# Kernel optimization log

Measured on AMD Instinct MI355X. Metric: run time of the kernel, lower is better.

Reference implementation:

```python
import jax, jax.numpy as jnp
import numpy as np

N_V = 250        # n_vertices (hardcoded in module)
NUM_WS = 14
W_DIM = 512
Z_DIM = 512
B = 64
E_PER = 1488     # ~directed convex-hull edges per graph (3N-6 undirected)
LR = 0.01        # lr_multiplier
CAM_R = 1.3


def _fc(x, w, b):
    # StyleGAN FullyConnectedLayer: runtime weight gain lr/sqrt(fan_in), bias gain lr,
    # bias_act 'lrelu' (alpha=0.2) with gain sqrt(2).
    gain = LR / np.sqrt(w.shape[1])
    y = x @ (w.T * gain) + b * LR
    return jax.nn.leaky_relu(y, 0.2) * np.sqrt(2.0)


def _seg_mean(vals, idx, n):
    s = jax.ops.segment_sum(vals, idx, num_segments=n)
    c = jax.ops.segment_sum(jnp.ones((idx.shape[0], 1), vals.dtype), idx, num_segments=n)
    return s / jnp.maximum(c, 1.0)


def _processor(x, edge_index, edge_attr, ew0, eb0, ew1, eb1, nw0, nb0, nw1, nb1, out_dim):
    src, dst = edge_index[0], edge_index[1]
    # edge encoder on [x_recv, x_send, edge_attr]
    ef = jnp.concatenate([x[src], x[dst], edge_attr], axis=-1)
    ef = _fc(_fc(ef, ew0, eb0), ew1, eb1)
    # PyG propagate (flow source_to_target): message = cat([x_i, edge_attr]) with
    # x_i = x[edge_index[1]], mean-aggregated onto edge_index[1].
    msg = jnp.concatenate([x[dst], ef], axis=-1)
    agg = _seg_mean(msg, dst, x.shape[0])
    nf = jnp.concatenate([x, agg[:, out_dim:]], axis=-1)
    nf = _fc(_fc(nf, nw0, nb0), nw1, nb1)
    return nf, ef


def setup_inputs() -> dict:
    key = jax.random.key(0)
    ks = jax.random.split(key, 24)
    z = jax.random.normal(ks[0], (B, Z_DIM), jnp.float32)
    la = jax.random.normal(ks[1], (B * N_V, 3), jnp.float32)
    look_ats = -CAM_R * la / jnp.linalg.norm(la, axis=-1, keepdims=True)
    # block-structured edges: each graph's edges stay within its 250-node block
    rng = np.random.default_rng(0)
    base = np.repeat(np.arange(B, dtype=np.int32) * N_V, E_PER)
    src = base + rng.integers(0, N_V, size=B * E_PER).astype(np.int32)
    dst = base + rng.integers(0, N_V, size=B * E_PER).astype(np.int32)
    edge_index = jnp.asarray(np.stack([src, dst]))
    # FullyConnectedLayer weights: init N(0,1)/lr_multiplier, bias 0
    def w(k, o, i):
        return jax.random.normal(k, (o, i), jnp.float32) / LR
    D = W_DIM
    inp = dict(z=z, look_ats=look_ats, edge_index=edge_index)
    inp.update(
        p0_ew0=w(ks[2], D, 1034), p0_eb0=jnp.zeros((D,), jnp.float32),
        p0_ew1=w(ks[3], D, D),    p0_eb1=jnp.zeros((D,), jnp.float32),
        p0_nw0=w(ks[4], D, 1030), p0_nb0=jnp.zeros((D,), jnp.float32),
        p0_nw1=w(ks[5], D, D),    p0_nb1=jnp.zeros((D,), jnp.float32),
        p1_ew0=w(ks[6], D, 1536), p1_eb0=jnp.zeros((D,), jnp.float32),
        p1_ew1=w(ks[7], D, D),    p1_eb1=jnp.zeros((D,), jnp.float32),
        p1_nw0=w(ks[8], D, 1024), p1_nb0=jnp.zeros((D,), jnp.float32),
        p1_nw1=w(ks[9], D, D),    p1_nb1=jnp.zeros((D,), jnp.float32),
    )
    return inp


def reference(z, look_ats, edge_index,
              p0_ew0, p0_eb0, p0_ew1, p0_eb1, p0_nw0, p0_nb0, p0_nw1, p0_nb1,
              p1_ew0, p1_eb0, p1_ew1, p1_eb1, p1_nw0, p1_nb0, p1_nw1, p1_nb1):
    b = z.shape[0]
    # normalize_2nd_moment
    zn = z * jax.lax.rsqrt(jnp.mean(jnp.square(z), axis=-1, keepdims=True) + 1e-8)
    # generate_graph: x = cat([z.repeat(N,1), look_ats]); edge_attr from look_ats
    x = jnp.concatenate([jnp.tile(zn, (N_V, 1)), look_ats], axis=-1)  # [B*N, 515]
    rel = look_ats[edge_index[1]] - look_ats[edge_index[0]]
    dist = jnp.linalg.norm(rel, axis=-1, keepdims=True)
    ea = jnp.concatenate([rel, dist], axis=-1)  # [E, 4]
    x, ea = _processor(x, edge_index, ea, p0_ew0, p0_eb0, p0_ew1, p0_eb1,
                       p0_nw0, p0_nb0, p0_nw1, p0_nb1, W_DIM)
    x, ea = _processor(x, edge_index, ea, p1_ew0, p1_eb0, p1_ew1, p1_eb1,
                       p1_nw0, p1_nb0, p1_nw1, p1_nb1, W_DIM)
    ws = x[::N_V]                        # in_ids = [i*N for i in range(B)]
    return jnp.tile(ws[:, None, :], (1, NUM_WS, 1))  # [B, num_ws, w_dim]
```

## Files before the change

kernel.cpp:

```cpp
#include <hip/hip_runtime.h>
#include <hip/hip_bf16.h>
#include <cmath>

#define NVP 250
#define NN  16000
#define EN  95232
#define LRc 0.01f
#define SQ2 1.41421356237309515f

#define CAP_ES 1024
#define CAP_N1 1024
#define CAP_E0 4096
#define EBLK ((EN + 255) / 256)
#define NBLK ((NN + 255) / 256)
#define SK_T 4

typedef __attribute__((ext_vector_type(8))) short bf16x8;
typedef __attribute__((ext_vector_type(4))) float f32x4;

__device__ __forceinline__ unsigned short bfc(float x) {
  unsigned u = __builtin_bit_cast(unsigned, x);
  u = (u + 0x7fffu + ((u >> 16) & 1u)) >> 16;
  return (unsigned short)u;
}
__device__ __forceinline__ unsigned pk2(float a, float b) {
  return (unsigned)bfc(a) | ((unsigned)bfc(b) << 16);
}

struct FEP {
  const float* bias; float gain;
  const float* T0p; const float* la; const float* cnt; const float* w0n;
  const int* rmap; const int* dst; const int* posN;
  float* outp; float* atomp;
};

template<int EPI>
__device__ __forceinline__ void mfma_epi(const FEP& f, f32x4 acc0, f32x4 acc1,
                                         f32x4 acc2, f32x4 acc3,
                                         int mBase, int nBase, int M,
                                         int lane, int wv) {
  const int fcol = lane & 15;
  int rows[4]; bool rok[4]; int tr[4];
  int rr4[4]; float la0[4], la1[4], la2[4]; bool has[4];
#pragma unroll
  for (int r = 0; r < 4; r++) {
    int row = mBase + wv*16 + (lane >> 4)*4 + r;
    rows[r] = row; rok[r] = row < M;
    int rc = rok[r] ? row : 0;
    if (EPI == 1) tr[r] = f.posN[f.dst[f.rmap[rc]]];
    if (EPI == 2) tr[r] = f.dst[f.rmap[rc]] / NVP;
    if (EPI == 7) {
      int nd = f.rmap[rc];
      rr4[r] = nd & 63;
      la0[r] = f.la[nd*3]; la1[r] = f.la[nd*3+1]; la2[r] = f.la[nd*3+2];
      has[r] = f.cnt[nd] > 0.f;
    }
  }
  f32x4 accs[4] = {acc0, acc1, acc2, acc3};
#pragma unroll
  for (int c = 0; c < 4; c++) {
    int n = nBase + fcol + 16*c;
    float bi = f.bias[n] * LRc;
    float w6[6];
    if (EPI == 7) {
#pragma unroll
      for (int j = 0; j < 6; j++) w6[j] = f.w0n[j*512 + n];
    }
#pragma unroll
    for (int r = 0; r < 4; r++) {
      if (!rok[r]) continue;
      float yr = accs[c][r];
      if (EPI == 7) {
#pragma unroll
        for (int zz = 0; zz < SK_T; zz++)
          yr += f.T0p[((size_t)zz*64 + rr4[r])*512 + n];
        float corr = la0[r]*w6[0] + la1[r]*w6[1] + la2[r]*w6[2];
        if (has[r]) corr += la0[r]*w6[3] + la1[r]*w6[4] + la2[r]*w6[5];
        yr += corr;
      }
      float y = yr * f.gain + bi;
      y = (y > 0.f ? y : 0.2f*y) * SQ2;
      if (EPI == 0 || EPI == 7) {
        f.outp[(size_t)rows[r]*512 + n] = y;
      } else if (EPI == 1) {
        f.outp[(size_t)rows[r]*512 + n] = y;
        atomicAdd(&f.atomp[(size_t)tr[r]*512 + n], y);
      } else {
        atomicAdd(&f.atomp[(size_t)tr[r]*512 + n], y);
      }
    }
  }
}

struct GMF {
  const float* W; const float* Ain; const int* Mdev;
  const float* cnt; const int* listN1;
  int Wld, Woff, Astride, K, Mcap, Mfix;
  FEP f;
};

template<int VECW, int SCALED, int EPI>
__global__ __launch_bounds__(256) void gemmMF(GMF p) {
  int M = p.Mdev ? *p.Mdev : p.Mfix;
  if (M > p.Mcap) M = p.Mcap;
  const int mBase = blockIdx.x * 64;
  if (mBase >= M) return;
  const int nBase = blockIdx.y * 64;

  __shared__ unsigned short Abf[64*72];
  __shared__ unsigned short Wbf[64*72];
  const int t = threadIdx.x;
  const int srow = t >> 2, sq = (t & 3) * 16;
  int arow = mBase + srow; if (arow >= M) arow = M - 1;
  float s = 1.f;
  if (SCALED) s = 1.0f / fmaxf(p.cnt[p.listN1[arow]], 1.0f);
  const float* aRow = p.Ain + (size_t)arow * p.Astride + sq;
  const float* wRow = p.W + (size_t)(nBase + srow) * p.Wld + p.Woff + sq;

  float4 ra[4], rw[4];
  auto ld = [&](int kt) {
#pragma unroll
    for (int i = 0; i < 4; i++) {
      ra[i] = *(const float4*)(aRow + kt + 4*i);
      if (VECW) {
        rw[i] = *(const float4*)(wRow + kt + 4*i);
      } else {
        const float* wp = wRow + kt + 4*i;
        rw[i] = make_float4(wp[0], wp[1], wp[2], wp[3]);
      }
    }
  };
  ld(0);

  const int lane = t & 63, wv = t >> 6;
  const int fr = wv*16 + (lane & 15);
  const int fcol = (lane & 15);
  const int fo = (lane >> 4) * 8;
  f32x4 acc0 = {}, acc1 = {}, acc2 = {}, acc3 = {};

  for (int kt = 0; kt < p.K; kt += 64) {
    if (kt > 0) __syncthreads();
    unsigned short* da = &Abf[srow*72 + sq];
    unsigned short* dw = &Wbf[srow*72 + sq];
#pragma unroll
    for (int i = 0; i < 4; i++) {
      uint2 ua; ua.x = pk2(ra[i].x*s, ra[i].y*s); ua.y = pk2(ra[i].z*s, ra[i].w*s);
      *(uint2*)&da[i*4] = ua;
      uint2 uw; uw.x = pk2(rw[i].x, rw[i].y); uw.y = pk2(rw[i].z, rw[i].w);
      *(uint2*)&dw[i*4] = uw;
    }
    __syncthreads();
    if (kt + 64 < p.K) ld(kt + 64);
#pragma unroll
    for (int kk = 0; kk < 64; kk += 32) {
      bf16x8 a = *(const bf16x8*)&Abf[fr*72 + kk + fo];
      bf16x8 b0 = *(const bf16x8*)&Wbf[( 0 + fcol)*72 + kk + fo];
      bf16x8 b1 = *(const bf16x8*)&Wbf[(16 + fcol)*72 + kk + fo];
      bf16x8 b2 = *(const bf16x8*)&Wbf[(32 + fcol)*72 + kk + fo];
      bf16x8 b3 = *(const bf16x8*)&Wbf[(48 + fcol)*72 + kk + fo];
      acc0 = __builtin_amdgcn_mfma_f32_16x16x32_bf16(a, b0, acc0, 0, 0, 0);
      acc1 = __builtin_amdgcn_mfma_f32_16x16x32_bf16(a, b1, acc1, 0, 0, 0);
      acc2 = __builtin_amdgcn_mfma_f32_16x16x32_bf16(a, b2, acc2, 0, 0, 0);
      acc3 = __builtin_amdgcn_mfma_f32_16x16x32_bf16(a, b3, acc3, 0, 0, 0);
    }
  }
  mfma_epi<EPI>(p.f, acc0, acc1, acc2, acc3, mBase, nBase, M, lane, wv);
}

struct GGS {
  const float* W; const float* x1c; const float* ef0c;
  const int* listES; const int* src; const int* dst; const int* posN; const int* posOf;
  const int* Mdev; float* pbuf; int KC;
};
__global__ __launch_bounds__(256) void gemmGS(GGS p) {
  int M = *p.Mdev; if (M > CAP_ES) M = CAP_ES;
  const int mBase = blockIdx.x * 64;
  if (mBase >= M) return;
  const int nBase = blockIdx.y * 64;
  const int z = blockIdx.z;
  int kBeg = z * p.KC, kEnd = kBeg + p.KC;

  __shared__ unsigned short Abf[64*72];
  __shared__ unsigned short Wbf[64*72];
  const int t = threadIdx.x;
  const int srow = t >> 2, sq = (t & 3) * 16;
  int arow = mBase + srow; if (arow >= M) arow = M - 1;
  int e = p.listES[arow];
  const float* s0 = p.x1c + (size_t)p.posN[p.src[e]] * 512;
  const float* s1 = p.x1c + (size_t)p.posN[p.dst[e]] * 512;
  const float* s2 = p.ef0c + (size_t)p.posOf[e] * 512;
  const float* wRow = p.W + (size_t)(nBase + srow) * 1536 + sq;

  float4 ra[4], rw[4];
  auto ld = [&](int kt) {
    int ka = kt + sq;
    const float* ap = (ka < 512) ? (s0 + ka) : (ka < 1024) ? (s1 + ka - 512)
                                                           : (s2 + ka - 1024);
#pragma unroll
    for (int i = 0; i < 4; i++) {
      ra[i] = *(const float4*)(ap + 4*i);
      rw[i] = *(const float4*)(wRow + kt + 4*i);
    }
  };
  ld(kBeg);

  const int lane = t & 63, wv = t >> 6;
  const int fr = wv*16 + (lane & 15);
  const int fcol = (lane & 15);
  const int fo = (lane >> 4) * 8;
  f32x4 acc0 = {}, acc1 = {}, acc2 = {}, acc3 = {};

  for (int kt = kBeg; kt < kEnd; kt += 64) {
    if (kt > kBeg) __syncthreads();
    unsigned short* da = &Abf[srow*72 + sq];
    unsigned short* dw = &Wbf[srow*72 + sq];
#pragma unroll
    for (int i = 0; i < 4; i++) {
      uint2 ua; ua.x = pk2(ra[i].x, ra[i].y); ua.y = pk2(ra[i].z, ra[i].w);
      *(uint2*)&da[i*4] = ua;
      uint2 uw; uw.x = pk2(rw[i].x, rw[i].y); uw.y = pk2(rw[i].z, rw[i].w);
      *(uint2*)&dw[i*4] = uw;
    }
    __syncthreads();
    if (kt + 64 < kEnd) ld(kt + 64);
#pragma unroll
    for (int kk = 0; kk < 64; kk += 32) {
      bf16x8 a = *(const bf16x8*)&Abf[fr*72 + kk + fo];
      bf16x8 b0 = *(const bf16x8*)&Wbf[( 0 + fcol)*72 + kk + fo];
      bf16x8 b1 = *(const bf16x8*)&Wbf[(16 + fcol)*72 + kk + fo];
      bf16x8 b2 = *(const bf16x8*)&Wbf[(32 + fcol)*72 + kk + fo];
      bf16x8 b3 = *(const bf16x8*)&Wbf[(48 + fcol)*72 + kk + fo];
      acc0 = __builtin_amdgcn_mfma_f32_16x16x32_bf16(a, b0, acc0, 0, 0, 0);
      acc1 = __builtin_amdgcn_mfma_f32_16x16x32_bf16(a, b1, acc1, 0, 0, 0);
      acc2 = __builtin_amdgcn_mfma_f32_16x16x32_bf16(a, b2, acc2, 0, 0, 0);
      acc3 = __builtin_amdgcn_mfma_f32_16x16x32_bf16(a, b3, acc3, 0, 0, 0);
    }
  }
  float* ob = p.pbuf + (size_t)z * CAP_ES * 512;
  int orow = mBase + wv*16 + (lane >> 4) * 4;
  int oc = nBase + fcol;
#pragma unroll
  for (int r = 0; r < 4; r++) {
    float* q = ob + (size_t)(orow + r) * 512 + oc;
    q[0] = acc0[r]; q[16] = acc1[r]; q[32] = acc2[r]; q[48] = acc3[r];
  }
}

struct EPS {
  const float* pbuf; const float* bias; const int* Mdev;
  float* outp; int SK; float gain;
};
__global__ __launch_bounds__(256) void epiS_k(EPS e) {
  int M = *e.Mdev; if (M > CAP_ES) M = CAP_ES;
  int i = blockIdx.x*256 + threadIdx.x;
  if (i >= M*128) return;
  int m = i >> 7, n4 = (i & 127) * 4;
  float ys[4] = {0.f, 0.f, 0.f, 0.f};
  for (int z = 0; z < e.SK; z++) {
    float4 v = *(const float4*)&e.pbuf[((size_t)z*CAP_ES + m)*512 + n4];
    ys[0] += v.x; ys[1] += v.y; ys[2] += v.z; ys[3] += v.w;
  }
#pragma unroll
  for (int j = 0; j < 4; j++) {
    float y = ys[j] * e.gain + e.bias[n4+j] * LRc;
    ys[j] = (y > 0.f ? y : 0.2f*y) * SQ2;
  }
  *(float4*)&e.outp[(size_t)m*512 + n4] = make_float4(ys[0],ys[1],ys[2],ys[3]);
}

template<int VECW, int NSEG>
__device__ __forceinline__ void gemm_loop(
    const float* const* b0, const float* const* b1,
    const float* sc0, const float* sc1,
    const float* w0, const float* w1, const float* w2, const float* w3,
    int kBeg, int kEnd,
    float (*As)[36], float (*Bs)[68], float acc[4][4]) {
  const int t = threadIdx.x;
  const int k4 = (t & 7) * 4;
  const int mr = t >> 3;
  const int tx = t & 15, ty = t >> 4;
  float4 ra0, ra1, rw0, rw1, rw2, rw3;
  auto lA = [&](int k0) {
    int ka = k0 + k4;
    int idx = 0;
    if (NSEG >= 2 && ka >= 512) idx = 1;
    if (NSEG == 3 && ka >= 1024) idx = 2;
    float s0 = sc0[idx], s1 = sc1[idx];
    ra0 = *(const float4*)(b0[idx] + ka);
    ra1 = *(const float4*)(b1[idx] + ka);
    ra0.x *= s0; ra0.y *= s0; ra0.z *= s0; ra0.w *= s0;
    ra1.x *= s1; ra1.y *= s1; ra1.z *= s1; ra1.w *= s1;
  };
  auto lW = [&](int k0) {
    if (VECW) {
      rw0 = *(const float4*)(w0 + k0); rw1 = *(const float4*)(w1 + k0);
      rw2 = *(const float4*)(w2 + k0); rw3 = *(const float4*)(w3 + k0);
    } else {
      rw0 = make_float4(w0[k0], w0[k0+1], w0[k0+2], w0[k0+3]);
      rw1 = make_float4(w1[k0], w1[k0+1], w1[k0+2], w1[k0+3]);
      rw2 = make_float4(w2[k0], w2[k0+1], w2[k0+2], w2[k0+3]);
      rw3 = make_float4(w3[k0], w3[k0+1], w3[k0+2], w3[k0+3]);
    }
  };
  lA(kBeg); lW(kBeg);
  for (int k0 = kBeg; k0 < kEnd; k0 += 32) {
    if (k0 > kBeg) __syncthreads();
    As[k4+0][mr] = ra0.x; As[k4+1][mr] = ra0.y;
    As[k4+2][mr] = ra0.z; As[k4+3][mr] = ra0.w;
    As[k4+0][mr+16] = ra1.x; As[k4+1][mr+16] = ra1.y;
    As[k4+2][mr+16] = ra1.z; As[k4+3][mr+16] = ra1.w;
    Bs[k4+0][mr]    = rw0.x; Bs[k4+1][mr]    = rw0.y; Bs[k4+2][mr]    = rw0.z; Bs[k4+3][mr]    = rw0.w;
    Bs[k4+0][mr+16] = rw1.x; Bs[k4+1][mr+16] = rw1.y; Bs[k4+2][mr+16] = rw1.z; Bs[k4+3][mr+16] = rw1.w;
    Bs[k4+0][mr+32] = rw2.x; Bs[k4+1][mr+32] = rw2.y; Bs[k4+2][mr+32] = rw2.z; Bs[k4+3][mr+32] = rw2.w;
    Bs[k4+0][mr+48] = rw3.x; Bs[k4+1][mr+48] = rw3.y; Bs[k4+2][mr+48] = rw3.z; Bs[k4+3][mr+48] = rw3.w;
    __syncthreads();
    if (k0 + 32 < kEnd) { lA(k0 + 32); lW(k0 + 32); }
#pragma unroll
    for (int kk = 0; kk < 32; kk++) {
      float4 a4 = *(const float4*)&As[kk][ty*4];
      float4 b4 = *(const float4*)&Bs[kk][tx*4];
      float aa[4] = {a4.x, a4.y, a4.z, a4.w};
      float bb[4] = {b4.x, b4.y, b4.z, b4.w};
#pragma unroll
      for (int i = 0; i < 4; i++)
#pragma unroll
        for (int j = 0; j < 4; j++) acc[i][j] += aa[i]*bb[j];
    }
  }
}

struct GTP {
  const float* W; const float* x1c; const float* agg1c; const float* cnt;
  const int* posN; float* pbuf; int KC;
};
__global__ __launch_bounds__(128) void gemmT(GTP p) {
  const int mBase = blockIdx.x * 32;
  const int nBase = blockIdx.y * 64;
  const int z = blockIdx.z;
  int kBeg = z * p.KC, kEnd = kBeg + p.KC;
  __shared__ float As[32][36];
  __shared__ float Bs[32][68];
  const int t = threadIdx.x;
  int r0 = mBase + (t>>3), r1 = r0 + 16;
  const float* b0[2] = { p.x1c + (size_t)p.posN[r0*NVP]*512,
                         p.agg1c + (size_t)r0*512 - 512 };
  const float* b1[2] = { p.x1c + (size_t)p.posN[r1*NVP]*512,
                         p.agg1c + (size_t)r1*512 - 512 };
  float sc0[2] = {1.f, 1.0f / fmaxf(p.cnt[r0*NVP], 1.0f)};
  float sc1[2] = {1.f, 1.0f / fmaxf(p.cnt[r1*NVP], 1.0f)};
  const int kofs = (t & 7)*4;
  const float* w0 = p.W + (size_t)(nBase + (t>>3)) * 1024 + kofs;
  const float* w1 = w0 + (size_t)16 * 1024;
  const float* w2 = w0 + (size_t)32 * 1024;
  const float* w3 = w0 + (size_t)48 * 1024;
  float acc[4][4] = {};
  gemm_loop<1, 2>(b0, b1, sc0, sc1, w0, w1, w2, w3, kBeg, kEnd, As, Bs, acc);
  const int tx = t & 15, ty = t >> 4;
#pragma unroll
  for (int i = 0; i < 4; i++) {
    int r = mBase + ty*4 + i;
    *(float4*)&p.pbuf[((size_t)z*64 + r)*512 + nBase + tx*4] =
      make_float4(acc[i][0],acc[i][1],acc[i][2],acc[i][3]);
  }
}

struct GPP {
  const float* W; const float* Ain; float* pbuf; int KC;
};
__global__ __launch_bounds__(128) void gemmP(GPP p) {
  const int mBase = blockIdx.x * 32;
  const int nBase = blockIdx.y * 64;
  const int z = blockIdx.z;
  int kBeg = z * p.KC, kEnd = kBeg + p.KC;
  __shared__ float As[32][36];
  __shared__ float Bs[32][68];
  const int t = threadIdx.x;
  const float* b0[1]; const float* b1[1]; float sc0[1] = {1.f}, sc1[1] = {1.f};
  b0[0] = p.Ain + (size_t)(mBase + (t>>3)) * 512;
  b1[0] = b0[0] + (size_t)16 * 512;
  const int kofs = (t & 7)*4;
  const float* w0 = p.W + (size_t)(nBase + (t>>3)) * 512 + kofs;
  const float* w1 = w0 + (size_t)16 * 512;
  const float* w2 = w0 + (size_t)32 * 512;
  const float* w3 = w0 + (size_t)48 * 512;
  float acc[4][4] = {};
  gemm_loop<1, 1>(b0, b1, sc0, sc1, w0, w1, w2, w3, kBeg, kEnd, As, Bs, acc);
  const int tx = t & 15, ty = t >> 4;
#pragma unroll
  for (int i = 0; i < 4; i++) {
    int r = mBase + ty*4 + i;
    *(float4*)&p.pbuf[((size_t)z*64 + r)*512 + nBase + tx*4] =
      make_float4(acc[i][0],acc[i][1],acc[i][2],acc[i][3]);
  }
}

struct EPP {
  const float* pbuf; const float* bias;
  float* outp; int SK; float gain;
};
template<int EPI>
__global__ __launch_bounds__(256) void epi_k(EPP e) {
  int i = blockIdx.x*256 + threadIdx.x;
  if (i >= 64*128) return;
  int m = i >> 7, n4 = (i & 127) * 4;
  float ys[4] = {0.f, 0.f, 0.f, 0.f};
  for (int z = 0; z < e.SK; z++) {
    float4 v = *(const float4*)&e.pbuf[((size_t)z*64 + m)*512 + n4];
    ys[0] += v.x; ys[1] += v.y; ys[2] += v.z; ys[3] += v.w;
  }
#pragma unroll
  for (int j = 0; j < 4; j++) {
    float y = ys[j] * e.gain + e.bias[n4+j] * LRc;
    ys[j] = (y > 0.f ? y : 0.2f*y) * SQ2;
  }
  float4 ov = make_float4(ys[0], ys[1], ys[2], ys[3]);
  if (EPI == 0) {
    *(float4*)&e.outp[(size_t)m*512 + n4] = ov;
  } else {
#pragma unroll
    for (int w = 0; w < 14; w++)
      *(float4*)&e.outp[((size_t)(m*14 + w))*512 + n4] = ov;
  }
}

struct TABP { const float* zn; const float* We; const float* Wn;
              float* pbTs; float* pbTd; float* pbT0; };
__global__ __launch_bounds__(128) void tab_k(TABP q) {
  int wsel = blockIdx.y >> 3;
  int nBase = (blockIdx.y & 7) * 64;
  const float* W = (wsel == 2) ? q.Wn : q.We;
  int Wld = (wsel == 2) ? 1030 : 1034;
  int Woff = (wsel == 1) ? 515 : 0;
  float* pb = (wsel == 0) ? q.pbTs : (wsel == 1) ? q.pbTd : q.pbT0;
  int z = blockIdx.z;
  __shared__ float As[32][36];
  __shared__ float Bs[32][68];
  const int t = threadIdx.x;
  const int mBase = blockIdx.x * 32;
  const float* b0[1]; const float* b1[1]; float sc0[1] = {1.f}, sc1[1] = {1.f};
  b0[0] = q.zn + (size_t)(mBase + (t>>3)) * 512;
  b1[0] = b0[0] + 16*512;
  const int kofs = (t & 7)*4 + Woff;
  const float* w0 = W + (size_t)(nBase + (t>>3)) * Wld + kofs;
  const float* w1 = w0 + (size_t)16 * Wld;
  const float* w2 = w0 + (size_t)32 * Wld;
  const float* w3 = w0 + (size_t)48 * Wld;
  float acc[4][4] = {};
  gemm_loop<0, 1>(b0, b1, sc0, sc1, w0, w1, w2, w3, z*128, z*128+128, As, Bs, acc);
  const int tx = t & 15, ty = t >> 4;
#pragma unroll
  for (int i = 0; i < 4; i++) {
    int r = mBase + ty*4 + i;
    *(float4*)&pb[((size_t)z*64 + r)*512 + nBase + tx*4] =
      make_float4(acc[i][0],acc[i][1],acc[i][2],acc[i][3]);
  }
}

__global__ __launch_bounds__(256) void init_k(const float* z, float* zn, int* need,
                                              const float* W0, const float* Wn,
                                              float* w0s, float* w0n) {
  int b = blockIdx.x, t = threadIdx.x;
  if (b < 64) {
    float s = 0.f;
    for (int j = t; j < 512; j += 256) { float v = z[b*512+j]; s += v*v; }
    for (int o = 32; o > 0; o >>= 1) s += __shfl_down(s, o);
    __shared__ float red[5];
    if ((t & 63) == 0) red[t >> 6] = s;
    __syncthreads();
    if (t == 0) {
      float tot = red[0]+red[1]+red[2]+red[3];
      red[4] = 1.0f / sqrtf(tot * (1.0f/512.0f) + 1e-8f);
    }
    __syncthreads();
    float r = red[4];
    for (int j = t; j < 512; j += 256) zn[b*512+j] = z[b*512+j] * r;
  } else if (b < 127) {
    int n = (b-64)*256 + t;
    if (n < NN) need[n] = ((n % NVP) == 0) ? 1 : 0;
  } else {
    int c = (b-127)*256 + t;
    const float* row = W0 + (size_t)c*1034;
    w0s[0*512+c] = row[512];  w0s[1*512+c] = row[513];  w0s[2*512+c] = row[514];
    w0s[3*512+c] = row[1027]; w0s[4*512+c] = row[1028]; w0s[5*512+c] = row[1029];
    w0s[6*512+c] = row[1030]; w0s[7*512+c] = row[1031]; w0s[8*512+c] = row[1032];
    w0s[9*512+c] = row[1033];
    const float* rn = Wn + (size_t)c*1030;
#pragma unroll
    for (int j = 0; j < 6; j++) w0n[j*512+c] = rn[512+j];
  }
}

__device__ __forceinline__ int blockCount(int pred, int* ws4) {
  unsigned long long m = __ballot(pred);
  int lane = threadIdx.x & 63, w = threadIdx.x >> 6;
  if (lane == 0) ws4[w] = __popcll(m);
  __syncthreads();
  return ws4[0] + ws4[1] + ws4[2] + ws4[3];
}
__device__ __forceinline__ int blockRank(int pred, int* ws4) {
  unsigned long long m = __ballot(pred);
  int lane = threadIdx.x & 63, w = threadIdx.x >> 6;
  if (lane == 0) ws4[w] = __popcll(m);
  __syncthreads();
  int off = 0;
  for (int i = 0; i < w; i++) off += ws4[i];
  return off + __popcll(m & ((1ull << lane) - 1ull));
}
__device__ __forceinline__ int blockSumN(const int* arr, int n, int* red) {
  int local = 0;
  for (int i = threadIdx.x; i < n; i += 256) local += arr[i];
  for (int o = 32; o > 0; o >>= 1) local += __shfl_down(local, o);
  if ((threadIdx.x & 63) == 0) red[threadIdx.x >> 6] = local;
  __syncthreads();
  int s = red[0]+red[1]+red[2]+red[3];
  __syncthreads();
  return s;
}

__global__ __launch_bounds__(256) void cntES_k(const int* src, const int* dst,
                                               float* cnt, int* need, int* bcnt) {
  __shared__ int ws4[4];
  int e = blockIdx.x*256 + threadIdx.x;
  int pred = 0;
  if (e < EN) {
    int d = dst[e];
    atomicAdd(&cnt[d], 1.0f);
    pred = (d % NVP) == 0;
    if (pred) need[src[e]] = 1;
  }
  int c = blockCount(pred, ws4);
  if (threadIdx.x == 0) bcnt[blockIdx.x] = c;
}
__global__ __launch_bounds__(256) void cntE0N1_k(const int* dst, const int* need,
                                                 int* bcntE, int* bcntN) {
  __shared__ int ws4[4];
  int b = blockIdx.x;
  if (b < EBLK) {
    int e = b*256 + threadIdx.x;
    int pred = (e < EN) && need[dst[e]];
    int c = blockCount(pred, ws4);
    if (threadIdx.x == 0) bcntE[b] = c;
  } else {
    int n = (b-EBLK)*256 + threadIdx.x;
    int pred = (n < NN) && need[n];
    int c = blockCount(pred, ws4);
    if (threadIdx.x == 0) bcntN[b-EBLK] = c;
  }
}
__global__ __launch_bounds__(256) void emit3s_k(const int* src, const int* dst,
                                                const int* need,
                                                const int* bcntS, int* listES,
                                                const int* bcntE, int* listE0, int* posOf,
                                                const int* bcntN, int* listN1, int* posN,
                                                int* tot) {
  __shared__ int red[4];
  __shared__ int ws4[4];
  int b = blockIdx.x;
  const int* bcnt; int bl, nblk, seg;
  if (b < EBLK)        { seg = 0; bl = b;          bcnt = bcntS; nblk = EBLK; }
  else if (b < 2*EBLK) { seg = 1; bl = b - EBLK;   bcnt = bcntE; nblk = EBLK; }
  else                 { seg = 2; bl = b - 2*EBLK; bcnt = bcntN; nblk = NBLK; }
  int boff = blockSumN(bcnt, bl, red);
  if (bl == 0) {
    int tt = blockSumN(bcnt, nblk, red);
    if (threadIdx.x == 0) tot[seg] = tt;
  }
  if (seg == 0) {
    int e = bl*256 + threadIdx.x;
    int pred = (e < EN) && (dst[e] % NVP == 0);
    int rank = blockRank(pred, ws4);
    if (pred) { int pos = boff + rank; if (pos < CAP_ES) listES[pos] = e; }
  } else if (seg == 1) {
    int e = bl*256 + threadIdx.x;
    int pred = (e < EN) && need[dst[e]];
    int rank = blockRank(pred, ws4);
    if (pred) { int pos = boff + rank;
      if (pos < CAP_E0) { listE0[pos] = e; posOf[e] = pos; } }
  } else {
    int n = bl*256 + threadIdx.x;
    int pred = (n < NN) && need[n];
    int rank = blockRank(pred, ws4);
    if (pred) { int pos = boff + rank;
      if (pos < CAP_N1) { listN1[pos] = n; posN[n] = pos; } }
  }
}

__global__ __launch_bounds__(128) void edge0_k(const int* nE0p, const int* listE0,
                                               const int* src, const int* dst,
                                               const float* pbTs, const float* pbTd,
                                               const float* la, const float* w0s,
                                               const float* b0, float* h0c) {
  int i = blockIdx.x;
  int n0 = *nE0p; if (n0 > CAP_E0) n0 = CAP_E0;
  if (i >= n0) return;
  int tid = threadIdx.x;
  int e = listE0[i];
  int s = src[e], d = dst[e];
  float a0 = la[s*3], a1 = la[s*3+1], a2 = la[s*3+2];
  float c0 = la[d*3], c1 = la[d*3+1], c2 = la[d*3+2];
  float r0 = c0-a0, r1 = c1-a1, r2 = c2-a2;
  float dn = sqrtf(r0*r0 + r1*r1 + r2*r2);
  const float g = LRc / 32.1558704423f;
  int sr = s & 63, dr = d & 63;
  int c4 = tid*4;
  float ys[4] = {0.f,0.f,0.f,0.f};
#pragma unroll
  for (int z = 0; z < SK_T; z++) {
    float4 vs = *(const float4*)&pbTs[((size_t)z*64 + sr)*512 + c4];
    float4 vd = *(const float4*)&pbTd[((size_t)z*64 + dr)*512 + c4];
    ys[0] += vs.x + vd.x; ys[1] += vs.y + vd.y;
    ys[2] += vs.z + vd.z; ys[3] += vs.w + vd.w;
  }
  float cf[10] = {a0,a1,a2,c0,c1,c2,r0,r1,r2,dn};
#pragma unroll
  for (int j = 0; j < 10; j++) {
    float4 wv = *(const float4*)&w0s[j*512 + c4];
    ys[0] += cf[j]*wv.x; ys[1] += cf[j]*wv.y; ys[2] += cf[j]*wv.z; ys[3] += cf[j]*wv.w;
  }
  float4 bv = *(const float4*)&b0[c4];
  float bb[4] = {bv.x, bv.y, bv.z, bv.w};
#pragma unroll
  for (int j = 0; j < 4; j++) {
    float y = ys[j]*g + bb[j]*LRc;
    ys[j] = (y > 0.f ? y : 0.2f*y) * SQ2;
  }
  *(float4*)&h0c[(size_t)i*512 + c4] = make_float4(ys[0],ys[1],ys[2],ys[3]);
}

extern "C" void kernel_launch(void* const* d_in, const int* in_sizes, int n_in,
                              void* d_out, int out_size, void* d_ws, size_t ws_size,
                              hipStream_t stream) {
  const float* z     = (const float*)d_in[0];
  const float* la    = (const float*)d_in[1];
  const int*   ei    = (const int*)  d_in[2];
  const float* p0ew0 = (const float*)d_in[3];
  const float* p0eb0 = (const float*)d_in[4];
  const float* p0ew1 = (const float*)d_in[5];
  const float* p0eb1 = (const float*)d_in[6];
  const float* p0nw0 = (const float*)d_in[7];
  const float* p0nb0 = (const float*)d_in[8];
  const float* p0nw1 = (const float*)d_in[9];
  const float* p0nb1 = (const float*)d_in[10];
  const float* p1ew0 = (const float*)d_in[11];
  const float* p1eb0 = (const float*)d_in[12];
  const float* p1ew1 = (const float*)d_in[13];
  const float* p1eb1 = (const float*)d_in[14];
  const float* p1nw0 = (const float*)d_in[15];
  const float* p1nb0 = (const float*)d_in[16];
  const float* p1nw1 = (const float*)d_in[17];
  const float* p1nb1 = (const float*)d_in[18];
  const int* src = ei;
  const int* dst = ei + EN;

  char* ws = (char*)d_ws;
  size_t off = 0;
  auto al = [&](size_t bytes) -> void* {
    void* r = (void*)(ws + off);
    off += (bytes + 255) & ~(size_t)255;
    return r;
  };
  float* cnt    = (float*)al(NN*4);
  float* agg0c  = (float*)al((size_t)CAP_N1*512*4);
  float* agg1c  = (float*)al(64*512*4);
  size_t zEnd = off;
  int*   tot    = (int*)  al(3*4);
  int*   need   = (int*)  al(NN*4);
  int*   posN   = (int*)  al(NN*4);
  int*   posOf  = (int*)  al((size_t)EN*4);
  int*   bcntS  = (int*)  al(EBLK*4);
  int*   bcntE  = (int*)  al(EBLK*4);
  int*   bcntN  = (int*)  al(NBLK*4);
  int*   listES = (int*)  al(CAP_ES*4);
  int*   listN1 = (int*)  al(CAP_N1*4);
  int*   listE0 = (int*)  al(CAP_E0*4);
  float* zn     = (float*)al(64*512*4);
  float* w0s    = (float*)al(10*512*4);
  float* w0n    = (float*)al(6*512*4);
  float* pbTs   = (float*)al((size_t)SK_T*64*512*4);
  float* pbTd   = (float*)al((size_t)SK_T*64*512*4);
  float* pbT0   = (float*)al((size_t)SK_T*64*512*4);
  float* h0c    = (float*)al((size_t)CAP_E0*512*4);
  float* ef0c   = (float*)al((size_t)CAP_E0*512*4);
  float* hn1    = (float*)al((size_t)CAP_N1*512*4);
  float* x1c    = (float*)al((size_t)CAP_N1*512*4);
  float* hs     = (float*)al((size_t)CAP_ES*512*4);
  float* hn64   = (float*)al(64*512*4);
  float* pbuf   = (float*)al((size_t)6*CAP_ES*512*4);

  hipMemsetAsync(ws, 0, zEnd, stream);

  init_k<<<129, 256, 0, stream>>>(z, zn, need, p0ew0, p0nw0, w0s, w0n);
  cntES_k<<<EBLK, 256, 0, stream>>>(src, dst, cnt, need, bcntS);
  cntE0N1_k<<<EBLK+NBLK, 256, 0, stream>>>(dst, need, bcntE, bcntN);
  emit3s_k<<<2*EBLK+NBLK, 256, 0, stream>>>(src, dst, need, bcntS, listES,
                                            bcntE, listE0, posOf,
                                            bcntN, listN1, posN, tot);
  {
    TABP q{zn, p0ew0, p0nw0, pbTs, pbTd, pbT0};
    tab_k<<<dim3(2, 24, SK_T), 128, 0, stream>>>(q);
  }
  edge0_k<<<CAP_E0, 128, 0, stream>>>(tot+1, listE0, src, dst, pbTs, pbTd, la, w0s,
                                      p0eb0, h0c);

  {
    GMF p{}; p.W = p0ew1; p.Wld = 512; p.Woff = 0; p.Astride = 512;
    p.K = 512; p.Mcap = CAP_E0; p.Mdev = tot+1; p.Ain = h0c;
    p.f.bias = p0eb1; p.f.gain = LRc/sqrtf(512.f);
    p.f.rmap = listE0; p.f.dst = dst; p.f.posN = posN;
    p.f.outp = ef0c; p.f.atomp = agg0c;
    gemmMF<1,0,1><<<dim3(CAP_E0/64, 8), 256, 0, stream>>>(p);
  }
  {
    GMF p{}; p.W = p0nw0; p.Wld = 1030; p.Woff = 518; p.Astride = 512;
    p.K = 512; p.Mcap = CAP_N1; p.Mdev = tot+2;
    p.Ain = agg0c; p.cnt = cnt; p.listN1 = listN1;
    p.f.bias = p0nb0; p.f.gain = LRc/sqrtf(1030.f);
    p.f.T0p = pbT0; p.f.la = la; p.f.cnt = cnt; p.f.w0n = w0n; p.f.rmap = listN1;
    p.f.outp = hn1;
    gemmMF<0,1,7><<<dim3(CAP_N1/64, 8), 256, 0, stream>>>(p);
  }
  {
    GMF p{}; p.W = p0nw1; p.Wld = 512; p.Woff = 0; p.Astride = 512;
    p.K = 512; p.Mcap = CAP_N1; p.Mdev = tot+2; p.Ain = hn1;
    p.f.bias = p0nb1; p.f.gain = LRc/sqrtf(512.f); p.f.outp = x1c;
    gemmMF<1,0,0><<<dim3(CAP_N1/64, 8), 256, 0, stream>>>(p);
  }
  {
    GGS p{}; p.W = p1ew0; p.x1c = x1c; p.ef0c = ef0c;
    p.listES = listES; p.src = src; p.dst = dst; p.posN = posN; p.posOf = posOf;
    p.Mdev = tot+0; p.pbuf = pbuf; p.KC = 256;
    gemmGS<<<dim3(CAP_ES/64, 8, 6), 256, 0, stream>>>(p);
    EPS e{}; e.pbuf = pbuf; e.SK = 6; e.Mdev = tot+0;
    e.bias = p1eb0; e.gain = LRc/sqrtf(1536.f); e.outp = hs;
    epiS_k<<<(CAP_ES*128)/256, 256, 0, stream>>>(e);
  }
  {
    GMF p{}; p.W = p1ew1; p.Wld = 512; p.Woff = 0; p.Astride = 512;
    p.K = 512; p.Mcap = CAP_ES; p.Mdev = tot+0; p.Ain = hs;
    p.f.bias = p1eb1; p.f.gain = LRc/sqrtf(512.f);
    p.f.rmap = listES; p.f.dst = dst; p.f.atomp = agg1c;
    gemmMF<1,0,2><<<dim3(CAP_ES/64, 8), 256, 0, stream>>>(p);
  }
  {
    GTP p{}; p.W = p1nw0; p.x1c = x1c; p.agg1c = agg1c; p.cnt = cnt;
    p.posN = posN; p.pbuf = pbuf; p.KC = 128;
    gemmT<<<dim3(2, 8, 8), 128, 0, stream>>>(p);
    EPP e{}; e.pbuf = pbuf; e.SK = 8; e.bias = p1nb0;
    e.gain = LRc/sqrtf(1024.f); e.outp = hn64;
    epi_k<0><<<(64*128)/256, 256, 0, stream>>>(e);
  }
  {
    GPP p{}; p.W = p1nw1; p.Ain = hn64; p.pbuf = pbuf; p.KC = 128;
    gemmP<<<dim3(2, 8, 4), 128, 0, stream>>>(p);
    EPP e{}; e.pbuf = pbuf; e.SK = 4; e.bias = p1nb1;
    e.gain = LRc/sqrtf(512.f); e.outp = (float*)d_out;
    epi_k<8><<<(64*128)/256, 256, 0, stream>>>(e);
  }
}
```

Baseline: 137.4 us.

## Fuse split-K reduction epilogue into next GEMM A-load and merge count kernel into init

The separate split-K reduction/activation kernel after gemmGS is removed. The following gemmMF now sums the six partial buffers, applies bias and leaky-relu while loading its A operand, and the intermediate hs buffer is dropped. The edge-count kernel is also folded into init_k as extra blocks, and `need` moves into the zeroed memset region so only the marked entries are written. This removes two launches and one round trip of the intermediate through memory. In exchange, each of the 8 column blocks redundantly re-reads six partial tiles per A load.

```diff
diff --git a/kernel.cpp b/kernel.cpp
--- a/kernel.cpp
+++ b/kernel.cpp
@@ -95,11 +95,12 @@
 struct GMF {
   const float* W; const float* Ain; const int* Mdev;
   const float* cnt; const int* listN1;
+  const float* pbufA; const float* biasA; float gainA; int SKA;
   int Wld, Woff, Astride, K, Mcap, Mfix;
   FEP f;
 };
 
-template<int VECW, int SCALED, int EPI>
+template<int VECW, int SCALED, int EPI, int AF>
 __global__ __launch_bounds__(256) void gemmMF(GMF p) {
   int M = p.Mdev ? *p.Mdev : p.Mfix;
   if (M > p.Mcap) M = p.Mcap;
@@ -121,7 +122,22 @@
   auto ld = [&](int kt) {
 #pragma unroll
     for (int i = 0; i < 4; i++) {
-      ra[i] = *(const float4*)(aRow + kt + 4*i);
+      if (AF) {
+        int col = kt + sq + 4*i;
+        float4 sm = make_float4(0.f, 0.f, 0.f, 0.f);
+        for (int zz = 0; zz < p.SKA; zz++) {
+          float4 v = *(const float4*)&p.pbufA[((size_t)zz*p.Mcap + arow)*512 + col];
+          sm.x += v.x; sm.y += v.y; sm.z += v.z; sm.w += v.w;
+        }
+        float4 bv = *(const float4*)&p.biasA[col];
+        float y;
+        y = sm.x*p.gainA + bv.x*LRc; ra[i].x = (y > 0.f ? y : 0.2f*y)*SQ2;
+        y = sm.y*p.gainA + bv.y*LRc; ra[i].y = (y > 0.f ? y : 0.2f*y)*SQ2;
+        y = sm.z*p.gainA + bv.z*LRc; ra[i].z = (y > 0.f ? y : 0.2f*y)*SQ2;
+        y = sm.w*p.gainA + bv.w*LRc; ra[i].w = (y > 0.f ? y : 0.2f*y)*SQ2;
+      } else {
+        ra[i] = *(const float4*)(aRow + kt + 4*i);
+      }
       if (VECW) {
         rw[i] = *(const float4*)(wRow + kt + 4*i);
       } else {
@@ -244,28 +260,6 @@
     float* q = ob + (size_t)(orow + r) * 512 + oc;
     q[0] = acc0[r]; q[16] = acc1[r]; q[32] = acc2[r]; q[48] = acc3[r];
   }
-}
-
-struct EPS {
-  const float* pbuf; const float* bias; const int* Mdev;
-  float* outp; int SK; float gain;
-};
-__global__ __launch_bounds__(256) void epiS_k(EPS e) {
-  int M = *e.Mdev; if (M > CAP_ES) M = CAP_ES;
-  int i = blockIdx.x*256 + threadIdx.x;
-  if (i >= M*128) return;
-  int m = i >> 7, n4 = (i & 127) * 4;
-  float ys[4] = {0.f, 0.f, 0.f, 0.f};
-  for (int z = 0; z < e.SK; z++) {
-    float4 v = *(const float4*)&e.pbuf[((size_t)z*CAP_ES + m)*512 + n4];
-    ys[0] += v.x; ys[1] += v.y; ys[2] += v.z; ys[3] += v.w;
-  }
-#pragma unroll
-  for (int j = 0; j < 4; j++) {
-    float y = ys[j] * e.gain + e.bias[n4+j] * LRc;
-    ys[j] = (y > 0.f ? y : 0.2f*y) * SQ2;
-  }
-  *(float4*)&e.outp[(size_t)m*512 + n4] = make_float4(ys[0],ys[1],ys[2],ys[3]);
 }
 
 template<int VECW, int NSEG>
@@ -456,9 +450,39 @@
   }
 }
 
+__device__ __forceinline__ int blockCount(int pred, int* ws4) {
+  unsigned long long m = __ballot(pred);
+  int lane = threadIdx.x & 63, w = threadIdx.x >> 6;
+  if (lane == 0) ws4[w] = __popcll(m);
+  __syncthreads();
+  return ws4[0] + ws4[1] + ws4[2] + ws4[3];
+}
+__device__ __forceinline__ int blockRank(int pred, int* ws4) {
+  unsigned long long m = __ballot(pred);
+  int lane = threadIdx.x & 63, w = threadIdx.x >> 6;
+  if (lane == 0) ws4[w] = __popcll(m);
+  __syncthreads();
+  int off = 0;
+  for (int i = 0; i < w; i++) off += ws4[i];
+  return off + __popcll(m & ((1ull << lane) - 1ull));
+}
+__device__ __forceinline__ int blockSumN(const int* arr, int n, int* red) {
+  int local = 0;
+  for (int i = threadIdx.x; i < n; i += 256) local += arr[i];
+  for (int o = 32; o > 0; o >>= 1) local += __shfl_down(local, o);
+  if ((threadIdx.x & 63) == 0) red[threadIdx.x >> 6] = local;
+  __syncthreads();
+  int s = red[0]+red[1]+red[2]+red[3];
+  __syncthreads();
+  return s;
+}
+
 __global__ __launch_bounds__(256) void init_k(const float* z, float* zn, int* need,
                                               const float* W0, const float* Wn,
-                                              float* w0s, float* w0n) {
+                                              float* w0s, float* w0n,
+                                              const int* src, const int* dst,
+                                              float* cnt, int* bcnt) {
+  __shared__ int ws4[4];
   int b = blockIdx.x, t = threadIdx.x;
   if (b < 64) {
     float s = 0.f;
@@ -476,8 +500,8 @@
     for (int j = t; j < 512; j += 256) zn[b*512+j] = z[b*512+j] * r;
   } else if (b < 127) {
     int n = (b-64)*256 + t;
-    if (n < NN) need[n] = ((n % NVP) == 0) ? 1 : 0;
-  } else {
+    if (n < NN && (n % NVP) == 0) need[n] = 1;
+  } else if (b < 129) {
     int c = (b-127)*256 + t;
     const float* row = W0 + (size_t)c*1034;
     w0s[0*512+c] = row[512];  w0s[1*512+c] = row[513];  w0s[2*512+c] = row[514];
@@ -487,50 +511,21 @@
     const float* rn = Wn + (size_t)c*1030;
 #pragma unroll
     for (int j = 0; j < 6; j++) w0n[j*512+c] = rn[512+j];
-  }
-}
-
-__device__ __forceinline__ int blockCount(int pred, int* ws4) {
-  unsigned long long m = __ballot(pred);
-  int lane = threadIdx.x & 63, w = threadIdx.x >> 6;
-  if (lane == 0) ws4[w] = __popcll(m);
-  __syncthreads();
-  return ws4[0] + ws4[1] + ws4[2] + ws4[3];
-}
-__device__ __forceinline__ int blockRank(int pred, int* ws4) {
-  unsigned long long m = __ballot(pred);
-  int lane = threadIdx.x & 63, w = threadIdx.x >> 6;
-  if (lane == 0) ws4[w] = __popcll(m);
-  __syncthreads();
-  int off = 0;
-  for (int i = 0; i < w; i++) off += ws4[i];
-  return off + __popcll(m & ((1ull << lane) - 1ull));
-}
-__device__ __forceinline__ int blockSumN(const int* arr, int n, int* red) {
-  int local = 0;
-  for (int i = threadIdx.x; i < n; i += 256) local += arr[i];
-  for (int o = 32; o > 0; o >>= 1) local += __shfl_down(local, o);
-  if ((threadIdx.x & 63) == 0) red[threadIdx.x >> 6] = local;
-  __syncthreads();
-  int s = red[0]+red[1]+red[2]+red[3];
-  __syncthreads();
-  return s;
-}
-
-__global__ __launch_bounds__(256) void cntES_k(const int* src, const int* dst,
-                                               float* cnt, int* need, int* bcnt) {
-  __shared__ int ws4[4];
-  int e = blockIdx.x*256 + threadIdx.x;
-  int pred = 0;
-  if (e < EN) {
-    int d = dst[e];
-    atomicAdd(&cnt[d], 1.0f);
-    pred = (d % NVP) == 0;
-    if (pred) need[src[e]] = 1;
-  }
-  int c = blockCount(pred, ws4);
-  if (threadIdx.x == 0) bcnt[blockIdx.x] = c;
-}
+  } else {
+    int bl = b - 129;
+    int e = bl*256 + t;
+    int pred = 0;
+    if (e < EN) {
+      int d = dst[e];
+      atomicAdd(&cnt[d], 1.0f);
+      pred = (d % NVP) == 0;
+      if (pred) need[src[e]] = 1;
+    }
+    int c = blockCount(pred, ws4);
+    if (t == 0) bcnt[bl] = c;
+  }
+}
+
 __global__ __launch_bounds__(256) void cntE0N1_k(const int* dst, const int* need,
                                                  int* bcntE, int* bcntN) {
   __shared__ int ws4[4];
@@ -660,11 +655,11 @@
     return r;
   };
   float* cnt    = (float*)al(NN*4);
+  int*   need   = (int*)  al(NN*4);
   float* agg0c  = (float*)al((size_t)CAP_N1*512*4);
   float* agg1c  = (float*)al(64*512*4);
   size_t zEnd = off;
   int*   tot    = (int*)  al(3*4);
-  int*   need   = (int*)  al(NN*4);
   int*   posN   = (int*)  al(NN*4);
   int*   posOf  = (int*)  al((size_t)EN*4);
   int*   bcntS  = (int*)  al(EBLK*4);
@@ -683,14 +678,13 @@
   float* ef0c   = (float*)al((size_t)CAP_E0*512*4);
   float* hn1    = (float*)al((size_t)CAP_N1*512*4);
   float* x1c    = (float*)al((size_t)CAP_N1*512*4);
-  float* hs     = (float*)al((size_t)CAP_ES*512*4);
   float* hn64   = (float*)al(64*512*4);
   float* pbuf   = (float*)al((size_t)6*CAP_ES*512*4);
 
   hipMemsetAsync(ws, 0, zEnd, stream);
 
-  init_k<<<129, 256, 0, stream>>>(z, zn, need, p0ew0, p0nw0, w0s, w0n);
-  cntES_k<<<EBLK, 256, 0, stream>>>(src, dst, cnt, need, bcntS);
+  init_k<<<129 + EBLK, 256, 0, stream>>>(z, zn, need, p0ew0, p0nw0, w0s, w0n,
+                                         src, dst, cnt, bcntS);
   cntE0N1_k<<<EBLK+NBLK, 256, 0, stream>>>(dst, need, bcntE, bcntN);
   emit3s_k<<<2*EBLK+NBLK, 256, 0, stream>>>(src, dst, need, bcntS, listES,
                                             bcntE, listE0, posOf,
@@ -708,7 +702,7 @@
     p.f.bias = p0eb1; p.f.gain = LRc/sqrtf(512.f);
     p.f.rmap = listE0; p.f.dst = dst; p.f.posN = posN;
     p.f.outp = ef0c; p.f.atomp = agg0c;
-    gemmMF<1,0,1><<<dim3(CAP_E0/64, 8), 256, 0, stream>>>(p);
+    gemmMF<1,0,1,0><<<dim3(CAP_E0/64, 8), 256, 0, stream>>>(p);
   }
   {
     GMF p{}; p.W = p0nw0; p.Wld = 1030; p.Woff = 518; p.Astride = 512;
@@ -717,29 +711,27 @@
     p.f.bias = p0nb0; p.f.gain = LRc/sqrtf(1030.f);
     p.f.T0p = pbT0; p.f.la = la; p.f.cnt = cnt; p.f.w0n = w0n; p.f.rmap = listN1;
     p.f.outp = hn1;
-    gemmMF<0,1,7><<<dim3(CAP_N1/64, 8), 256, 0, stream>>>(p);
+    gemmMF<0,1,7,0><<<dim3(CAP_N1/64, 8), 256, 0, stream>>>(p);
   }
   {
     GMF p{}; p.W = p0nw1; p.Wld = 512; p.Woff = 0; p.Astride = 512;
     p.K = 512; p.Mcap = CAP_N1; p.Mdev = tot+2; p.Ain = hn1;
     p.f.bias = p0nb1; p.f.gain = LRc/sqrtf(512.f); p.f.outp = x1c;
-    gemmMF<1,0,0><<<dim3(CAP_N1/64, 8), 256, 0, stream>>>(p);
+    gemmMF<1,0,0,0><<<dim3(CAP_N1/64, 8), 256, 0, stream>>>(p);
   }
   {
     GGS p{}; p.W = p1ew0; p.x1c = x1c; p.ef0c = ef0c;
     p.listES = listES; p.src = src; p.dst = dst; p.posN = posN; p.posOf = posOf;
     p.Mdev = tot+0; p.pbuf = pbuf; p.KC = 256;
     gemmGS<<<dim3(CAP_ES/64, 8, 6), 256, 0, stream>>>(p);
-    EPS e{}; e.pbuf = pbuf; e.SK = 6; e.Mdev = tot+0;
-    e.bias = p1eb0; e.gain = LRc/sqrtf(1536.f); e.outp = hs;
-    epiS_k<<<(CAP_ES*128)/256, 256, 0, stream>>>(e);
   }
   {
     GMF p{}; p.W = p1ew1; p.Wld = 512; p.Woff = 0; p.Astride = 512;
-    p.K = 512; p.Mcap = CAP_ES; p.Mdev = tot+0; p.Ain = hs;
+    p.K = 512; p.Mcap = CAP_ES; p.Mdev = tot+0;
+    p.pbufA = pbuf; p.biasA = p1eb0; p.gainA = LRc/sqrtf(1536.f); p.SKA = 6;
     p.f.bias = p1eb1; p.f.gain = LRc/sqrtf(512.f);
     p.f.rmap = listES; p.f.dst = dst; p.f.atomp = agg1c;
-    gemmMF<1,0,2><<<dim3(CAP_ES/64, 8), 256, 0, stream>>>(p);
+    gemmMF<1,0,2,1><<<dim3(CAP_ES/64, 8), 256, 0, stream>>>(p);
   }
   {
     GTP p{}; p.W = p1nw0; p.x1c = x1c; p.agg1c = agg1c; p.cnt = cnt;
```

Result: slower. 162.4 us (+18.2%).
